# Performance work log

Measured on AMD Instinct MI355X. Metric: run time of the kernel, lower is better.

The kernel has to match this reference:

```python
import jax, jax.numpy as jnp
import numpy as np

EMB_D, N_SLOTS, KEY_D, N_ITER = 768, 16, 64, 3
E_LAYERS, E_P_LEN = 5, 8
BS, N_TOK = 128, 196


def _ln(x, w, b, eps=1e-5):
    m = x.mean(-1, keepdims=True)
    v = ((x - m) ** 2).mean(-1, keepdims=True)
    return (x - m) / jnp.sqrt(v + eps) * w + b


def setup_inputs() -> dict:
    key = jax.random.key(0)
    ks = jax.random.split(key, 16)
    n = lambda k, *s: jax.random.normal(k, s, jnp.float32)
    u = lambda k, *s: jax.random.uniform(k, s, jnp.float32)
    return {
        "features": n(ks[0], BS, N_TOK, EMB_D),
        "slot_noise": n(ks[1], BS, N_SLOTS, KEY_D),
        "ln_in_w": jnp.ones((EMB_D,)), "ln_in_b": jnp.zeros((EMB_D,)),
        "ln_slot_w": jnp.ones((KEY_D,)), "ln_slot_b": jnp.zeros((KEY_D,)),
        "ln_out_w": jnp.ones((KEY_D,)), "ln_out_b": jnp.zeros((KEY_D,)),
        "mu": u(ks[2], KEY_D),
        "sigma": u(ks[3], KEY_D),
        "Wk": n(ks[4], EMB_D, KEY_D) * 0.02,   # stored as [in, out]
        "Wq": n(ks[5], KEY_D, KEY_D) * 0.02,
        "Wv": n(ks[6], EMB_D, KEY_D) * 0.02,
        "W_ih": n(ks[7], 3 * KEY_D, KEY_D) * 0.1,  # GRU input weights (r,z,n)
        "W_hh": n(ks[8], 3 * KEY_D, KEY_D) * 0.1,  # GRU hidden weights (r,z,n)
        "b_ih": jnp.zeros((3 * KEY_D,)), "b_hh": jnp.zeros((3 * KEY_D,)),
        "W1": n(ks[9], KEY_D, KEY_D) * 0.1, "b1": jnp.zeros((KEY_D,)),
        "W2": n(ks[10], KEY_D, KEY_D) * 0.1, "b2": jnp.zeros((KEY_D,)),
        "s2p": u(ks[11], KEY_D, E_LAYERS, E_P_LEN, EMB_D),
    }


def reference(features, slot_noise, ln_in_w, ln_in_b, ln_slot_w, ln_slot_b,
              ln_out_w, ln_out_b, mu, sigma, Wk, Wq, Wv,
              W_ih, W_hh, b_ih, b_hh, W1, b1, W2, b2, s2p):
    scale = KEY_D ** -0.5
    eps = 1e-8
    f = _ln(features, ln_in_w, ln_in_b)          # [b, n, emb_d]
    k = f @ Wk                                    # [b, n, d] (features fixed, so hoisted)
    v = f @ Wv                                    # [b, n, d]
    slots = slot_noise * sigma + mu               # [b, k, d]
    for _ in range(N_ITER):
        slots_prev = slots
        q = _ln(slots, ln_slot_w, ln_slot_b) @ Wq  # [b, k, d]
        attn = jnp.einsum('bnd,bkd->bnk', k, q) * scale
        attn = jax.nn.softmax(attn, axis=-1) + eps       # softmax over slots
        attn = attn / attn.sum(axis=-2, keepdims=True)   # renormalize over tokens
        updates = jnp.einsum('bnk,bnd->bkd', attn, v)    # [b, k, d]
        # single-step GRU cell (PyTorch gate order r, z, n)
        gi = updates @ W_ih.T + b_ih
        gh = slots_prev @ W_hh.T + b_hh
        ir, iz, inn = jnp.split(gi, 3, axis=-1)
        hr, hz, hn = jnp.split(gh, 3, axis=-1)
        r = jax.nn.sigmoid(ir + hr)
        z = jax.nn.sigmoid(iz + hz)
        ncand = jnp.tanh(inn + r * hn)
        slots = (1.0 - z) * ncand + z * slots_prev
        # residual MLP
        h = _ln(slots, ln_out_w, ln_out_b)
        slots = slots + jax.nn.relu(h @ W1.T + b1) @ W2.T + b2
    prompts = jnp.einsum('bkh,hepd->bkepd', slots, s2p)  # [b, k, 5, 8, emb_d]
    return prompts
```

## Files before the change

### kernel.cpp

```cpp
#include <hip/hip_runtime.h>
#include <hip/hip_bf16.h>

#define EMB_D   768
#define N_SLOTS 16
#define KEY_D   64
#define N_ITER  3
#define BS      128
#define N_TOK   196
#define N_ROWS  (BS * N_TOK)
#define PROMPT_N (5 * 8 * EMB_D)
#define TOT_SLOT_ROWS (BS * N_SLOTS)

typedef __attribute__((ext_vector_type(8))) short bf16x8;
typedef __attribute__((ext_vector_type(4))) float f32x4;

__device__ __forceinline__ float sigmoid_f(float x) { return 1.f / (1.f + __expf(-x)); }
__device__ __forceinline__ float tanh_f(float x)    { return 1.f - 2.f / (__expf(2.f * x) + 1.f); }
__device__ __forceinline__ short f2bf(float f) {
    __hip_bfloat16 h = __float2bfloat16(f);
    return *reinterpret_cast<short*>(&h);
}
__device__ __forceinline__ float bf2f(short s) {
    return __int_as_float(((int)(unsigned short)s) << 16);
}
__device__ __forceinline__ float dot4(float4 a, float4 b) {
    return a.x * b.x + a.y * b.y + a.z * b.z + a.w * b.w;
}

__global__ __launch_bounds__(256) void wprep_kernel(
    const float* __restrict__ Wk, const float* __restrict__ Wv,
    short* __restrict__ WT)
{
    const int idx = blockIdx.x * 256 + threadIdx.x;
    if (idx < 128 * 768) {
        const int n = idx / 768, k = idx % 768;
        const float v = (n < 64) ? Wk[(size_t)k * 64 + n] : Wv[(size_t)k * 64 + (n - 64)];
        WT[idx] = f2bf(v);
    }
}

__global__ __launch_bounds__(256) void gwprep_kernel(
    const float* __restrict__ W_ih, const float* __restrict__ W_hh,
    const float* __restrict__ W1, const float* __restrict__ W2,
    const float* __restrict__ Wq, short* __restrict__ WB)
{
    const int idx = blockIdx.x * 256 + threadIdx.x;
    if (idx < 576 * 64) {
        const int row = idx >> 6, d = idx & 63;
        float v;
        if      (row < 192) v = W_ih[(size_t)row * 64 + d];
        else if (row < 384) v = W_hh[(size_t)(row - 192) * 64 + d];
        else if (row < 448) v = W1[(size_t)(row - 384) * 64 + d];
        else if (row < 512) v = W2[(size_t)(row - 448) * 64 + d];
        else                v = Wq[(size_t)d * 64 + (row - 512)];
        WB[idx] = f2bf(v);
    }
}

__global__ __launch_bounds__(256) void pt_prep_kernel(
    const float* __restrict__ s2p, short* __restrict__ PT)
{
    const int n = blockIdx.x * 256 + threadIdx.x;
    short o[64];
    #pragma unroll
    for (int h = 0; h < 64; ++h)
        o[h] = f2bf(s2p[(size_t)h * PROMPT_N + n]);
    short* op = PT + (size_t)n * 64;
    #pragma unroll
    for (int j = 0; j < 8; ++j)
        *(bf16x8*)&op[j * 8] = *(const bf16x8*)&o[j * 8];
}

__global__ __launch_bounds__(256) void ln_bf16_kernel(
    const float* __restrict__ feat, const float* __restrict__ lnw,
    const float* __restrict__ lnb, short* __restrict__ fbuf)
{
    const int wave = threadIdx.x >> 6, lane = threadIdx.x & 63;
    const int row = blockIdx.x * 4 + wave;
    const float* fr = feat + (size_t)row * EMB_D + lane * 12;

    float x[12];
    #pragma unroll
    for (int j = 0; j < 3; ++j)
        *(float4*)&x[j * 4] = *(const float4*)&fr[j * 4];

    float s = 0.f, ss = 0.f;
    #pragma unroll
    for (int j = 0; j < 12; ++j) { s += x[j]; ss += x[j] * x[j]; }
    #pragma unroll
    for (int m = 32; m >= 1; m >>= 1) { s += __shfl_xor(s, m, 64); ss += __shfl_xor(ss, m, 64); }
    const float mean = s * (1.f / EMB_D);
    const float rstd = rsqrtf(ss * (1.f / EMB_D) - mean * mean + 1e-5f);

    const float* wp = lnw + lane * 12;
    const float* bp = lnb + lane * 12;
    short o[12];
    #pragma unroll
    for (int j = 0; j < 12; ++j)
        o[j] = f2bf((x[j] - mean) * rstd * wp[j] + bp[j]);

    short* op = fbuf + (size_t)row * EMB_D + lane * 12;
    #pragma unroll
    for (int j = 0; j < 3; ++j)
        *(short4*)&op[j * 4] = *(const short4*)&o[j * 4];
}

__global__ __launch_bounds__(256) void kvgemm_kernel(
    const short* __restrict__ fbuf, const short* __restrict__ WT,
    float* __restrict__ kbuf, float* __restrict__ vbuf)
{
    const int t = threadIdx.x;
    const int wave = t >> 6, lane = t & 63;
    const int rowbase = blockIdx.x * 64 + (wave & 1) * 32;
    const int colbase = (wave >> 1) * 64;
    const int lrow = lane & 15, lk = (lane >> 4) * 8;

    f32x4 acc[2][4];
    #pragma unroll
    for (int m = 0; m < 2; ++m)
        #pragma unroll
        for (int c = 0; c < 4; ++c)
            acc[m][c] = (f32x4){0.f, 0.f, 0.f, 0.f};

    const short* a0 = fbuf + (size_t)(rowbase + lrow) * EMB_D + lk;
    const short* a1 = a0 + 16 * EMB_D;
    const short* bp = WT + (size_t)(colbase + lrow) * EMB_D + lk;

    #pragma unroll 2
    for (int k0 = 0; k0 < EMB_D; k0 += 32) {
        const bf16x8 af0 = *(const bf16x8*)(a0 + k0);
        const bf16x8 af1 = *(const bf16x8*)(a1 + k0);
        #pragma unroll
        for (int c = 0; c < 4; ++c) {
            const bf16x8 bf = *(const bf16x8*)(bp + (size_t)c * 16 * EMB_D + k0);
            acc[0][c] = __builtin_amdgcn_mfma_f32_16x16x32_bf16(af0, bf, acc[0][c], 0, 0, 0);
            acc[1][c] = __builtin_amdgcn_mfma_f32_16x16x32_bf16(af1, bf, acc[1][c], 0, 0, 0);
        }
    }

    const int dn = lane & 15;
    const int dm0 = (lane >> 4) * 4;
    #pragma unroll
    for (int m = 0; m < 2; ++m) {
        #pragma unroll
        for (int c = 0; c < 4; ++c) {
            const int col = colbase + c * 16 + dn;
            float* outp = (col < 64) ? (kbuf + col) : (vbuf + col - 64);
            #pragma unroll
            for (int r = 0; r < 4; ++r) {
                const int row = rowbase + m * 16 + dm0 + r;
                outp[(size_t)row * 64] = acc[m][c][r];
            }
        }
    }
}

__global__ __launch_bounds__(512) void slot_iter_kernel(
    const float* __restrict__ kbuf, const float* __restrict__ vbuf,
    const short* __restrict__ WB,
    const float* __restrict__ noise, const float* __restrict__ mu,
    const float* __restrict__ sigma,
    const float* __restrict__ lnsw, const float* __restrict__ lnsb,
    const float* __restrict__ lnow, const float* __restrict__ lnob,
    const float* __restrict__ b_ih, const float* __restrict__ b_hh,
    const float* __restrict__ b1, const float* __restrict__ b2,
    short* __restrict__ slotsB)
{
    __shared__ float k_l[N_TOK][68];
    __shared__ short v_l[N_TOK][68];
    __shared__ float att[N_TOK][17];
    __shared__ float slots[16][68];
    __shared__ float snew[16][68];
    __shared__ float q_l[16][68];
    __shared__ float gi_l[16][204];
    __shared__ float gh_l[16][204];
    __shared__ float csp[32][17];
    __shared__ float cs_inv[16];
    __shared__ short lnb_bf[16][72];
    __shared__ short upd_bf[16][72];
    __shared__ short slots_bf[16][72];
    __shared__ short mlp_bf[16][72];

    const int b = blockIdx.x, t = threadIdx.x;
    const int wv = t >> 6, lane = t & 63;
    const int l15 = lane & 15, lk8 = (lane >> 4) * 8;
    const int dr0 = (lane >> 4) * 4;

    {
        const float* kb = kbuf + (size_t)b * N_TOK * 64;
        const float* vb = vbuf + (size_t)b * N_TOK * 64;
        for (int i4 = t; i4 < N_TOK * 16; i4 += 512) {
            const int r = i4 >> 4, c4 = (i4 & 15) * 4;
            *(float4*)&k_l[r][c4] = *(const float4*)&kb[r * 64 + c4];
            const float4 vx = *(const float4*)&vb[r * 64 + c4];
            short4 vs;
            vs.x = f2bf(vx.x); vs.y = f2bf(vx.y); vs.z = f2bf(vx.z); vs.w = f2bf(vx.w);
            *(short4*)&v_l[r][c4] = vs;
        }
    }

    if (t < 256) {
        const int s = t >> 4, d0 = (t & 15) * 4;
        const float4 nz = *(const float4*)&noise[((size_t)b * 16 + s) * 64 + d0];
        float x[4];
        x[0] = nz.x * sigma[d0 + 0] + mu[d0 + 0];
        x[1] = nz.y * sigma[d0 + 1] + mu[d0 + 1];
        x[2] = nz.z * sigma[d0 + 2] + mu[d0 + 2];
        x[3] = nz.w * sigma[d0 + 3] + mu[d0 + 3];
        #pragma unroll
        for (int k = 0; k < 4; ++k) {
            slots[s][d0 + k] = x[k];
            slots_bf[s][d0 + k] = f2bf(x[k]);
        }
        float sum = x[0] + x[1] + x[2] + x[3];
        float ssm = x[0]*x[0] + x[1]*x[1] + x[2]*x[2] + x[3]*x[3];
        #pragma unroll
        for (int m = 8; m >= 1; m >>= 1) { sum += __shfl_xor(sum, m, 64); ssm += __shfl_xor(ssm, m, 64); }
        const float mean = sum * (1.f / 64);
        const float rstd = rsqrtf(ssm * (1.f / 64) - mean * mean + 1e-5f);
        #pragma unroll
        for (int k = 0; k < 4; ++k)
            lnb_bf[s][d0 + k] = f2bf((x[k] - mean) * rstd * lnsw[d0 + k] + lnsb[d0 + k]);
    }
    __syncthreads();

    if (wv < 4) {
        const short* ar = &lnb_bf[l15][lk8];
        const short* br = WB + (size_t)(512 + wv * 16 + l15) * 64 + lk8;
        f32x4 acc = (f32x4){0.f, 0.f, 0.f, 0.f};
        acc = __builtin_amdgcn_mfma_f32_16x16x32_bf16(*(const bf16x8*)ar,
              *(const bf16x8*)br, acc, 0, 0, 0);
        acc = __builtin_amdgcn_mfma_f32_16x16x32_bf16(*(const bf16x8*)(ar + 32),
              *(const bf16x8*)(br + 32), acc, 0, 0, 0);
        const int col = wv * 16 + l15;
        #pragma unroll
        for (int r = 0; r < 4; ++r) q_l[dr0 + r][col] = acc[r] * 0.125f;
    }
    __syncthreads();

    for (int it = 0; it < N_ITER; ++it) {
        {
            const int s = t & 15, ng = t >> 4;
            float4 q4[16];
            #pragma unroll
            for (int dq = 0; dq < 16; ++dq) q4[dq] = *(const float4*)&q_l[s][dq * 4];
            float psum = 0.f;
            #pragma unroll
            for (int i = 0; i < 7; ++i) {
                const int n = ng + 32 * i;
                if (n < N_TOK) {
                    float a = 0.f;
                    #pragma unroll
                    for (int dq = 0; dq < 16; ++dq)
                        a += dot4(*(const float4*)&k_l[n][dq * 4], q4[dq]);
                    float mx = a;
                    #pragma unroll
                    for (int mm = 1; mm < 16; mm <<= 1) mx = fmaxf(mx, __shfl_xor(mx, mm, 64));
                    const float e = __expf(a - mx);
                    float sm = e;
                    #pragma unroll
                    for (int mm = 1; mm < 16; mm <<= 1) sm += __shfl_xor(sm, mm, 64);
                    const float av = e / sm + 1e-8f;
                    att[n][s] = av;
                    psum += av;
                }
            }
            csp[ng][s] = psum;
        }
        __syncthreads();
        if (t < 16) {
            float cs = 0.f;
            #pragma unroll
            for (int ng = 0; ng < 32; ++ng) cs += csp[ng][t];
            cs_inv[t] = 1.f / cs;
        }
        __syncthreads();

        {
            const int d2 = (t & 31) * 2, s = t >> 5;
            float a0 = 0.f, a1 = 0.f;
            #pragma unroll 4
            for (int n = 0; n < N_TOK; ++n) {
                const float an = att[n][s];
                const short2 v2 = *(const short2*)&v_l[n][d2];
                a0 = fmaf(an, bf2f(v2.x), a0);
                a1 = fmaf(an, bf2f(v2.y), a1);
            }
            const float ci = cs_inv[s];
            upd_bf[s][d2]     = f2bf(a0 * ci);
            upd_bf[s][d2 + 1] = f2bf(a1 * ci);
        }
        __syncthreads();

        {
            #pragma unroll
            for (int u = wv; u < 24; u += 8) {
                const int isgh = (u >= 12);
                const int tile = isgh ? u - 12 : u;
                const short* ar = isgh ? &slots_bf[l15][lk8] : &upd_bf[l15][lk8];
                const short* br = WB + (size_t)(isgh * 192 + tile * 16 + l15) * 64 + lk8;
                f32x4 acc = (f32x4){0.f, 0.f, 0.f, 0.f};
                acc = __builtin_amdgcn_mfma_f32_16x16x32_bf16(*(const bf16x8*)ar,
                      *(const bf16x8*)br, acc, 0, 0, 0);
                acc = __builtin_amdgcn_mfma_f32_16x16x32_bf16(*(const bf16x8*)(ar + 32),
                      *(const bf16x8*)(br + 32), acc, 0, 0, 0);
                float* dst = isgh ? &gh_l[0][0] : &gi_l[0][0];
                const int col = tile * 16 + l15;
                #pragma unroll
                for (int r = 0; r < 4; ++r) dst[(dr0 + r) * 204 + col] = acc[r];
            }
        }
        __syncthreads();

        if (t < 256) {
            const int s = t >> 4, d0 = t & 15;
            #pragma unroll
            for (int m = 0; m < 4; ++m) {
                const int d = d0 + 16 * m;
                const float r  = sigmoid_f(gi_l[s][d] + b_ih[d] + gh_l[s][d] + b_hh[d]);
                const float z  = sigmoid_f(gi_l[s][64 + d] + b_ih[64 + d] + gh_l[s][64 + d] + b_hh[64 + d]);
                const float nc = tanh_f(gi_l[s][128 + d] + b_ih[128 + d]
                                        + r * (gh_l[s][128 + d] + b_hh[128 + d]));
                snew[s][d] = (1.f - z) * nc + z * slots[s][d];
            }
        }
        __syncthreads();

        if (t < 256) {
            const int s = t >> 4, d0 = (t & 15) * 4;
            const float4 x = *(const float4*)&snew[s][d0];
            float sum = x.x + x.y + x.z + x.w;
            float ssm = x.x*x.x + x.y*x.y + x.z*x.z + x.w*x.w;
            #pragma unroll
            for (int m = 8; m >= 1; m >>= 1) { sum += __shfl_xor(sum, m, 64); ssm += __shfl_xor(ssm, m, 64); }
            const float mean = sum * (1.f / 64);
            const float rstd = rsqrtf(ssm * (1.f / 64) - mean * mean + 1e-5f);
            lnb_bf[s][d0 + 0] = f2bf((x.x - mean) * rstd * lnow[d0 + 0] + lnob[d0 + 0]);
            lnb_bf[s][d0 + 1] = f2bf((x.y - mean) * rstd * lnow[d0 + 1] + lnob[d0 + 1]);
            lnb_bf[s][d0 + 2] = f2bf((x.z - mean) * rstd * lnow[d0 + 2] + lnob[d0 + 2]);
            lnb_bf[s][d0 + 3] = f2bf((x.w - mean) * rstd * lnow[d0 + 3] + lnob[d0 + 3]);
        }
        __syncthreads();

        if (wv < 4) {
            const short* ar = &lnb_bf[l15][lk8];
            const short* br = WB + (size_t)(384 + wv * 16 + l15) * 64 + lk8;
            f32x4 acc = (f32x4){0.f, 0.f, 0.f, 0.f};
            acc = __builtin_amdgcn_mfma_f32_16x16x32_bf16(*(const bf16x8*)ar,
                  *(const bf16x8*)br, acc, 0, 0, 0);
            acc = __builtin_amdgcn_mfma_f32_16x16x32_bf16(*(const bf16x8*)(ar + 32),
                  *(const bf16x8*)(br + 32), acc, 0, 0, 0);
            const int col = wv * 16 + l15;
            const float bb = b1[col];
            #pragma unroll
            for (int r = 0; r < 4; ++r)
                mlp_bf[dr0 + r][col] = f2bf(fmaxf(acc[r] + bb, 0.f));
        }
        __syncthreads();

        if (wv < 4) {
            const short* ar = &mlp_bf[l15][lk8];
            const short* br = WB + (size_t)(448 + wv * 16 + l15) * 64 + lk8;
            f32x4 acc = (f32x4){0.f, 0.f, 0.f, 0.f};
            acc = __builtin_amdgcn_mfma_f32_16x16x32_bf16(*(const bf16x8*)ar,
                  *(const bf16x8*)br, acc, 0, 0, 0);
            acc = __builtin_amdgcn_mfma_f32_16x16x32_bf16(*(const bf16x8*)(ar + 32),
                  *(const bf16x8*)(br + 32), acc, 0, 0, 0);
            const int col = wv * 16 + l15;
            const float bb = b2[col];
            #pragma unroll
            for (int r = 0; r < 4; ++r) {
                const float v = snew[dr0 + r][col] + acc[r] + bb;
                slots[dr0 + r][col] = v;
                slots_bf[dr0 + r][col] = f2bf(v);
            }
        }
        __syncthreads();

        if (it < N_ITER - 1) {
            if (t < 256) {
                const int s = t >> 4, d0 = (t & 15) * 4;
                const float4 x = *(const float4*)&slots[s][d0];
                float sum = x.x + x.y + x.z + x.w;
                float ssm = x.x*x.x + x.y*x.y + x.z*x.z + x.w*x.w;
                #pragma unroll
                for (int m = 8; m >= 1; m >>= 1) { sum += __shfl_xor(sum, m, 64); ssm += __shfl_xor(ssm, m, 64); }
                const float mean = sum * (1.f / 64);
                const float rstd = rsqrtf(ssm * (1.f / 64) - mean * mean + 1e-5f);
                lnb_bf[s][d0 + 0] = f2bf((x.x - mean) * rstd * lnsw[d0 + 0] + lnsb[d0 + 0]);
                lnb_bf[s][d0 + 1] = f2bf((x.y - mean) * rstd * lnsw[d0 + 1] + lnsb[d0 + 1]);
                lnb_bf[s][d0 + 2] = f2bf((x.z - mean) * rstd * lnsw[d0 + 2] + lnsb[d0 + 2]);
                lnb_bf[s][d0 + 3] = f2bf((x.w - mean) * rstd * lnsw[d0 + 3] + lnsb[d0 + 3]);
            }
            __syncthreads();
            if (wv < 4) {
                const short* ar = &lnb_bf[l15][lk8];
                const short* br = WB + (size_t)(512 + wv * 16 + l15) * 64 + lk8;
                f32x4 acc = (f32x4){0.f, 0.f, 0.f, 0.f};
                acc = __builtin_amdgcn_mfma_f32_16x16x32_bf16(*(const bf16x8*)ar,
                      *(const bf16x8*)br, acc, 0, 0, 0);
                acc = __builtin_amdgcn_mfma_f32_16x16x32_bf16(*(const bf16x8*)(ar + 32),
                      *(const bf16x8*)(br + 32), acc, 0, 0, 0);
                const int col = wv * 16 + l15;
                #pragma unroll
                for (int r = 0; r < 4; ++r) q_l[dr0 + r][col] = acc[r] * 0.125f;
            }
            __syncthreads();
        }
    }

    for (int idx = t; idx < 1024; idx += 512)
        slotsB[(size_t)b * 1024 + idx] = slots_bf[idx >> 6][idx & 63];
}

__global__ __launch_bounds__(256) void prompt_mfma_kernel(
    const short* __restrict__ slotsB, const short* __restrict__ PT,
    float* __restrict__ out)
{
    __shared__ float stg[4][16][132];
    const int wave = threadIdx.x >> 6, lane = threadIdx.x & 63;
    const int rowblk = blockIdx.x & 127;
    const int colblk = blockIdx.x >> 7;
    const int rowbase = rowblk * 16;
    const int colbase = colblk * 512 + wave * 128;
    const int l15 = lane & 15, lk = (lane >> 4) * 8;

    const short* bp = slotsB + (size_t)(rowbase + l15) * 64 + lk;
    const bf16x8 b0 = *(const bf16x8*)bp;
    const bf16x8 b1 = *(const bf16x8*)(bp + 32);

    f32x4 acc[8];
    #pragma unroll
    for (int c = 0; c < 8; ++c) {
        const short* ap = PT + (size_t)(colbase + c * 16 + l15) * 64 + lk;
        const bf16x8 a0 = *(const bf16x8*)ap;
        const bf16x8 a1 = *(const bf16x8*)(ap + 32);
        acc[c] = (f32x4){0.f, 0.f, 0.f, 0.f};
        acc[c] = __builtin_amdgcn_mfma_f32_16x16x32_bf16(a0, b0, acc[c], 0, 0, 0);
        acc[c] = __builtin_amdgcn_mfma_f32_16x16x32_bf16(a1, b1, acc[c], 0, 0, 0);
    }

    const int nofs = (lane >> 4) * 4;
    #pragma unroll
    for (int c = 0; c < 8; ++c)
        *(f32x4*)&stg[wave][l15][c * 16 + nofs] = acc[c];

    const int rrow = lane >> 5;
    const int chunk = lane & 31;
    #pragma unroll
    for (int p = 0; p < 8; ++p) {
        const int row = p * 2 + rrow;
        const f32x4 v = *(const f32x4*)&stg[wave][row][chunk * 4];
        __builtin_nontemporal_store(
            v, (f32x4*)&out[(size_t)(rowbase + row) * PROMPT_N + colbase + chunk * 4]);
    }
}

extern "C" void kernel_launch(void* const* d_in, const int* in_sizes, int n_in,
                              void* d_out, int out_size, void* d_ws, size_t ws_size,
                              hipStream_t stream)
{
    (void)in_sizes; (void)n_in; (void)out_size; (void)ws_size;
    const float* feat    = (const float*)d_in[0];
    const float* noise   = (const float*)d_in[1];
    const float* ln_in_w = (const float*)d_in[2];
    const float* ln_in_b = (const float*)d_in[3];
    const float* ln_s_w  = (const float*)d_in[4];
    const float* ln_s_b  = (const float*)d_in[5];
    const float* ln_o_w  = (const float*)d_in[6];
    const float* ln_o_b  = (const float*)d_in[7];
    const float* mu      = (const float*)d_in[8];
    const float* sigma   = (const float*)d_in[9];
    const float* Wk      = (const float*)d_in[10];
    const float* Wq      = (const float*)d_in[11];
    const float* Wv      = (const float*)d_in[12];
    const float* W_ih    = (const float*)d_in[13];
    const float* W_hh    = (const float*)d_in[14];
    const float* b_ih    = (const float*)d_in[15];
    const float* b_hh    = (const float*)d_in[16];
    const float* W1      = (const float*)d_in[17];
    const float* b1      = (const float*)d_in[18];
    const float* W2      = (const float*)d_in[19];
    const float* b2      = (const float*)d_in[20];
    const float* s2p     = (const float*)d_in[21];

    float* kbuf   = (float*)d_ws;
    float* vbuf   = kbuf  + (size_t)N_ROWS * 64;
    short* slotsB = (short*)(vbuf + (size_t)N_ROWS * 64);
    short* PT     = slotsB + (size_t)TOT_SLOT_ROWS * KEY_D;
    short* fbuf   = PT + (size_t)PROMPT_N * KEY_D;
    short* WT     = fbuf + (size_t)N_ROWS * EMB_D;
    short* WB     = WT + (size_t)128 * EMB_D;

    hipLaunchKernelGGL(wprep_kernel, dim3((128 * 768 + 255) / 256), dim3(256), 0, stream,
                       Wk, Wv, WT);
    hipLaunchKernelGGL(gwprep_kernel, dim3((576 * 64 + 255) / 256), dim3(256), 0, stream,
                       W_ih, W_hh, W1, W2, Wq, WB);
    hipLaunchKernelGGL(pt_prep_kernel, dim3(PROMPT_N / 256), dim3(256), 0, stream,
                       s2p, PT);
    hipLaunchKernelGGL(ln_bf16_kernel, dim3(N_ROWS / 4), dim3(256), 0, stream,
                       feat, ln_in_w, ln_in_b, fbuf);
    hipLaunchKernelGGL(kvgemm_kernel, dim3(N_ROWS / 64), dim3(256), 0, stream,
                       fbuf, WT, kbuf, vbuf);
    hipLaunchKernelGGL(slot_iter_kernel, dim3(BS), dim3(512), 0, stream,
                       kbuf, vbuf, WB, noise, mu, sigma, ln_s_w, ln_s_b,
                       ln_o_w, ln_o_b, b_ih, b_hh, b1, b2, slotsB);
    hipLaunchKernelGGL(prompt_mfma_kernel, dim3(60 * 128), dim3(256), 0, stream,
                       slotsB, PT, (float*)d_out);
}
```

Baseline: 182.0 us.

## Merge weight prep kernels, process two rows per wave in LN, use plain stores

Folds the three weight-preparation kernels into one launch that dispatches on block index, which removes two kernel launches and their gaps. The input LayerNorm kernel now has each wave handle two rows, halving the grid and giving more loads in flight per thread. The prompt output kernel swaps nontemporal stores for ordinary stores, which changes how the large output write interacts with the cache. These are three unrelated tweaks, and the store change could help or hurt write bandwidth.

```diff
diff --git a/kernel.cpp b/kernel.cpp
--- a/kernel.cpp
+++ b/kernel.cpp
@@ -27,25 +27,24 @@
     return a.x * b.x + a.y * b.y + a.z * b.z + a.w * b.w;
 }
 
-__global__ __launch_bounds__(256) void wprep_kernel(
+#define WT_BLKS 384
+#define WB_BLKS 144
+#define PT_BLKS 120
+__global__ __launch_bounds__(256) void prep_kernel(
     const float* __restrict__ Wk, const float* __restrict__ Wv,
-    short* __restrict__ WT)
+    const float* __restrict__ W_ih, const float* __restrict__ W_hh,
+    const float* __restrict__ W1, const float* __restrict__ W2,
+    const float* __restrict__ Wq, const float* __restrict__ s2p,
+    short* __restrict__ WT, short* __restrict__ WB, short* __restrict__ PT)
 {
-    const int idx = blockIdx.x * 256 + threadIdx.x;
-    if (idx < 128 * 768) {
+    const int blk = blockIdx.x;
+    if (blk < WT_BLKS) {
+        const int idx = blk * 256 + threadIdx.x;
         const int n = idx / 768, k = idx % 768;
         const float v = (n < 64) ? Wk[(size_t)k * 64 + n] : Wv[(size_t)k * 64 + (n - 64)];
         WT[idx] = f2bf(v);
-    }
-}
-
-__global__ __launch_bounds__(256) void gwprep_kernel(
-    const float* __restrict__ W_ih, const float* __restrict__ W_hh,
-    const float* __restrict__ W1, const float* __restrict__ W2,
-    const float* __restrict__ Wq, short* __restrict__ WB)
-{
-    const int idx = blockIdx.x * 256 + threadIdx.x;
-    if (idx < 576 * 64) {
+    } else if (blk < WT_BLKS + WB_BLKS) {
+        const int idx = (blk - WT_BLKS) * 256 + threadIdx.x;
         const int row = idx >> 6, d = idx & 63;
         float v;
         if      (row < 192) v = W_ih[(size_t)row * 64 + d];
@@ -54,21 +53,17 @@
         else if (row < 512) v = W2[(size_t)(row - 448) * 64 + d];
         else                v = Wq[(size_t)d * 64 + (row - 512)];
         WB[idx] = f2bf(v);
-    }
-}
-
-__global__ __launch_bounds__(256) void pt_prep_kernel(
-    const float* __restrict__ s2p, short* __restrict__ PT)
-{
-    const int n = blockIdx.x * 256 + threadIdx.x;
-    short o[64];
-    #pragma unroll
-    for (int h = 0; h < 64; ++h)
-        o[h] = f2bf(s2p[(size_t)h * PROMPT_N + n]);
-    short* op = PT + (size_t)n * 64;
-    #pragma unroll
-    for (int j = 0; j < 8; ++j)
-        *(bf16x8*)&op[j * 8] = *(const bf16x8*)&o[j * 8];
+    } else {
+        const int n = (blk - WT_BLKS - WB_BLKS) * 256 + threadIdx.x;
+        short o[64];
+        #pragma unroll
+        for (int h = 0; h < 64; ++h)
+            o[h] = f2bf(s2p[(size_t)h * PROMPT_N + n]);
+        short* op = PT + (size_t)n * 64;
+        #pragma unroll
+        for (int j = 0; j < 8; ++j)
+            *(bf16x8*)&op[j * 8] = *(const bf16x8*)&o[j * 8];
+    }
 }
 
 __global__ __launch_bounds__(256) void ln_bf16_kernel(
@@ -76,33 +71,50 @@
     const float* __restrict__ lnb, short* __restrict__ fbuf)
 {
     const int wave = threadIdx.x >> 6, lane = threadIdx.x & 63;
-    const int row = blockIdx.x * 4 + wave;
-    const float* fr = feat + (size_t)row * EMB_D + lane * 12;
-
-    float x[12];
-    #pragma unroll
-    for (int j = 0; j < 3; ++j)
-        *(float4*)&x[j * 4] = *(const float4*)&fr[j * 4];
-
-    float s = 0.f, ss = 0.f;
-    #pragma unroll
-    for (int j = 0; j < 12; ++j) { s += x[j]; ss += x[j] * x[j]; }
-    #pragma unroll
-    for (int m = 32; m >= 1; m >>= 1) { s += __shfl_xor(s, m, 64); ss += __shfl_xor(ss, m, 64); }
-    const float mean = s * (1.f / EMB_D);
-    const float rstd = rsqrtf(ss * (1.f / EMB_D) - mean * mean + 1e-5f);
+    const int r0 = blockIdx.x * 8 + wave * 2;
+    const float* fr0 = feat + (size_t)r0 * EMB_D + lane * 12;
+    const float* fr1 = fr0 + EMB_D;
+
+    float x[12], y[12];
+    #pragma unroll
+    for (int j = 0; j < 3; ++j) {
+        *(float4*)&x[j * 4] = *(const float4*)&fr0[j * 4];
+        *(float4*)&y[j * 4] = *(const float4*)&fr1[j * 4];
+    }
+
+    float sx = 0.f, ssx = 0.f, sy = 0.f, ssy = 0.f;
+    #pragma unroll
+    for (int j = 0; j < 12; ++j) {
+        sx += x[j]; ssx += x[j] * x[j];
+        sy += y[j]; ssy += y[j] * y[j];
+    }
+    #pragma unroll
+    for (int m = 32; m >= 1; m >>= 1) {
+        sx += __shfl_xor(sx, m, 64); ssx += __shfl_xor(ssx, m, 64);
+        sy += __shfl_xor(sy, m, 64); ssy += __shfl_xor(ssy, m, 64);
+    }
+    const float mx = sx * (1.f / EMB_D);
+    const float rx = rsqrtf(ssx * (1.f / EMB_D) - mx * mx + 1e-5f);
+    const float my = sy * (1.f / EMB_D);
+    const float ry = rsqrtf(ssy * (1.f / EMB_D) - my * my + 1e-5f);
 
     const float* wp = lnw + lane * 12;
     const float* bp = lnb + lane * 12;
-    short o[12];
-    #pragma unroll
-    for (int j = 0; j < 12; ++j)
-        o[j] = f2bf((x[j] - mean) * rstd * wp[j] + bp[j]);
-
-    short* op = fbuf + (size_t)row * EMB_D + lane * 12;
-    #pragma unroll
-    for (int j = 0; j < 3; ++j)
-        *(short4*)&op[j * 4] = *(const short4*)&o[j * 4];
+    short ox[12], oy[12];
+    #pragma unroll
+    for (int j = 0; j < 12; ++j) {
+        const float w = wp[j], bb = bp[j];
+        ox[j] = f2bf((x[j] - mx) * rx * w + bb);
+        oy[j] = f2bf((y[j] - my) * ry * w + bb);
+    }
+
+    short* op0 = fbuf + (size_t)r0 * EMB_D + lane * 12;
+    short* op1 = op0 + EMB_D;
+    #pragma unroll
+    for (int j = 0; j < 3; ++j) {
+        *(short4*)&op0[j * 4] = *(const short4*)&ox[j * 4];
+        *(short4*)&op1[j * 4] = *(const short4*)&oy[j * 4];
+    }
 }
 
 __global__ __launch_bounds__(256) void kvgemm_kernel(
@@ -451,8 +463,7 @@
     for (int p = 0; p < 8; ++p) {
         const int row = p * 2 + rrow;
         const f32x4 v = *(const f32x4*)&stg[wave][row][chunk * 4];
-        __builtin_nontemporal_store(
-            v, (f32x4*)&out[(size_t)(rowbase + row) * PROMPT_N + colbase + chunk * 4]);
+        *(f32x4*)&out[(size_t)(rowbase + row) * PROMPT_N + colbase + chunk * 4] = v;
     }
 }
 
@@ -492,13 +503,9 @@
     short* WT     = fbuf + (size_t)N_ROWS * EMB_D;
     short* WB     = WT + (size_t)128 * EMB_D;
 
-    hipLaunchKernelGGL(wprep_kernel, dim3((128 * 768 + 255) / 256), dim3(256), 0, stream,
-                       Wk, Wv, WT);
-    hipLaunchKernelGGL(gwprep_kernel, dim3((576 * 64 + 255) / 256), dim3(256), 0, stream,
-                       W_ih, W_hh, W1, W2, Wq, WB);
-    hipLaunchKernelGGL(pt_prep_kernel, dim3(PROMPT_N / 256), dim3(256), 0, stream,
-                       s2p, PT);
-    hipLaunchKernelGGL(ln_bf16_kernel, dim3(N_ROWS / 4), dim3(256), 0, stream,
+    hipLaunchKernelGGL(prep_kernel, dim3(WT_BLKS + WB_BLKS + PT_BLKS), dim3(256), 0, stream,
+                       Wk, Wv, W_ih, W_hh, W1, W2, Wq, s2p, WT, WB, PT);
+    hipLaunchKernelGGL(ln_bf16_kernel, dim3(N_ROWS / 8), dim3(256), 0, stream,
                        feat, ln_in_w, ln_in_b, fbuf);
     hipLaunchKernelGGL(kvgemm_kernel, dim3(N_ROWS / 64), dim3(256), 0, stream,
                        fbuf, WT, kbuf, vbuf);
```

Result: slower. 194.6 us (+6.9%).
